# Optimization experiments

Measured on AMD Instinct MI355X. Metric: run time of the kernel, lower is better.

The kernel has to match this reference:

```python
import jax, jax.numpy as jnp
import numpy as np

K = 20
EPS = 1e-5

def _lrelu(x):
    return jnp.where(x >= 0, x, 0.2 * x)

def _bn(x, g, b, m, v, axis=1):
    shp = [1] * x.ndim
    shp[axis] = -1
    scale = (g / jnp.sqrt(v + EPS)).reshape(shp)
    return (x - m.reshape(shp)) * scale + b.reshape(shp)

def _graph_feature(x, k):
    # x: [B, C, N] -> [B, 2C, N, k]  (kNN in feature space, concat(x_j - x_i, x_i))
    xx = jnp.sum(x * x, axis=1)                        # [B, N]
    inner = jnp.einsum('bcn,bcm->bnm', x, x)           # [B, N, N]
    neg_dist = 2.0 * inner - xx[:, :, None] - xx[:, None, :]
    _, idx = jax.lax.top_k(neg_dist, k)                # [B, N, k] nearest neighbors
    xt = jnp.transpose(x, (0, 2, 1))                   # [B, N, C]
    nb = jax.vmap(lambda f, i: f[i])(xt, idx)          # [B, N, k, C]
    center = jnp.broadcast_to(xt[:, :, None, :], nb.shape)
    feat = jnp.concatenate([nb - center, center], axis=-1)  # [B, N, k, 2C]
    return jnp.transpose(feat, (0, 3, 1, 2))

def _edge_block(x, w, g, b, m, v):
    # EdgeConv: graph feature -> 1x1 conv -> BN -> LeakyReLU -> max over k
    f = _graph_feature(x, K)                           # [B, 2C, N, k]
    y = jnp.einsum('oc,bcnk->bonk', w, f)
    y = _lrelu(_bn(y, g, b, m, v, 1))
    return jnp.max(y, axis=-1)                         # [B, O, N]


def setup_inputs() -> dict:
    key = jax.random.key(0)
    ks = iter(jax.random.split(key, 64))
    def randn(*s, scale=1.0):
        return jax.random.normal(next(ks), s, dtype=jnp.float32) * scale
    def unif(*s):
        return jax.random.uniform(next(ks), s, dtype=jnp.float32, minval=0.5, maxval=1.5)
    d = {}
    d['x'] = randn(16, 3, 1024)
    # conv / linear weights (fan-in scaled)
    for name, o, c in [('w1', 64, 6), ('w2', 64, 128), ('w3', 128, 128),
                       ('w4', 256, 256), ('w5', 1024, 512),
                       ('wl1', 512, 2048), ('wl2', 256, 512), ('wl3', 101, 256)]:
        d[name] = randn(o, c, scale=1.0 / np.sqrt(c))
    d['bl2'] = randn(256, scale=0.02)
    d['bl3'] = randn(101, scale=0.02)
    # BN params (eval-mode running stats)
    for i, c in [('1', 64), ('2', 64), ('3', 128), ('4', 256), ('5', 1024), ('6', 512), ('7', 256)]:
        d['g' + i] = 1.0 + randn(c, scale=0.1)
        d['b' + i] = randn(c, scale=0.1)
        d['m' + i] = randn(c, scale=0.1)
        d['v' + i] = unif(c)
    return d


def reference(x, w1, g1, b1, m1, v1, w2, g2, b2, m2, v2, w3, g3, b3, m3, v3,
              w4, g4, b4, m4, v4, w5, g5, b5, m5, v5,
              wl1, g6, b6, m6, v6, wl2, bl2, g7, b7, m7, v7, wl3, bl3):
    x1 = _edge_block(x,  w1, g1, b1, m1, v1)   # [B, 64, N]
    x2 = _edge_block(x1, w2, g2, b2, m2, v2)   # [B, 64, N]
    x3 = _edge_block(x2, w3, g3, b3, m3, v3)   # [B, 128, N]
    x4 = _edge_block(x3, w4, g4, b4, m4, v4)   # [B, 256, N]
    xc = jnp.concatenate([x1, x2, x3, x4], axis=1)           # [B, 512, N]
    y = _lrelu(_bn(jnp.einsum('oc,bcn->bon', w5, xc), g5, b5, m5, v5, 1))  # [B, 1024, N]
    p = jnp.concatenate([jnp.max(y, axis=-1), jnp.mean(y, axis=-1)], axis=1)  # [B, 2048]
    h = _lrelu(_bn(p @ wl1.T, g6, b6, m6, v6, 1))            # [B, 512]
    h = _lrelu(_bn(h @ wl2.T + bl2, g7, b7, m7, v7, 1))      # [B, 256]
    return h @ wl3.T + bl3                                   # [B, 101]
```

## Files before the change

### kernel.cpp

```cpp
#include <hip/hip_runtime.h>
#include <cstdint>
#include <cmath>

#define DI __device__ __forceinline__

constexpr int BB = 16;
constexpr int NN = 1024;
constexpr int KK = 20;
constexpr int NPT = BB*NN;
constexpr float EPSF = 1e-5f;
constexpr float NEGINF = -3.0e38f;

DI float lrelu(float x){ return x >= 0.f ? x : 0.2f * x; }
DI float dot4(const float4 a, const float4 b){ return a.x*b.x + a.y*b.y + a.z*b.z + a.w*b.w; }
DI unsigned short f2bf(float x){
    uint32_t u = __float_as_uint(x);
    uint32_t r = (u + 0x7fffu + ((u >> 16) & 1u)) >> 16;
    return (unsigned short)r;
}

typedef __attribute__((ext_vector_type(8))) short short8v;
typedef __attribute__((ext_vector_type(4))) float f32x4;

__global__ void k_transpose(const float* __restrict__ x, float* __restrict__ xt)
{
    int i = blockIdx.x * 256 + threadIdx.x;
    if (i >= NPT) return;
    int b = i >> 10, n = i & 1023;
    #pragma unroll
    for (int c = 0; c < 3; ++c) xt[i*3 + c] = x[(b*3 + c)*NN + n];
}

__global__ void k_sqnorm(const float* __restrict__ src, int stride, int C, float* __restrict__ xx)
{
    int i = blockIdx.x * 256 + threadIdx.x;
    if (i >= NPT) return;
    const float* r = src + (size_t)i * stride;
    float s = 0.f;
    for (int c = 0; c < C; ++c){ float v = r[c]; s += v * v; }
    xx[i] = s;
}

template<int C>
__global__ __launch_bounds__(1024, 4) void k_knn(const float* __restrict__ src, int stride,
                                                 const float* __restrict__ xx,
                                                 int* __restrict__ idxo)
{
    constexpr bool SMALL = (C == 3);
    constexpr int CG = SMALL ? 1 : (C / 4);
    constexpr int TS = SMALL ? 5 : C;
    __shared__ float tile[128 * TS];

    const int tid  = threadIdx.x;
    const int lane = tid & 63;
    const int wv   = __builtin_amdgcn_readfirstlane(tid >> 6);
    const int b  = blockIdx.x >> 4;
    const int q0 = (blockIdx.x & 15) << 6;
    const int qbase = b*NN + q0 + (wv << 2);

    const float* qp0 = src + (size_t)(qbase + 0)*stride;
    const float* qp1 = src + (size_t)(qbase + 1)*stride;
    const float* qp2 = src + (size_t)(qbase + 2)*stride;
    const float* qp3 = src + (size_t)(qbase + 3)*stride;

    float xxq[4];
    #pragma unroll
    for (int q = 0; q < 4; ++q) xxq[q] = xx[qbase + q];

    float val[4][16];

    #pragma unroll
    for (int t = 0; t < 8; ++t){
        __syncthreads();
        if constexpr (SMALL){
            for (int i = tid; i < 128*3; i += 1024){
                int row = i / 3, c = i % 3;
                tile[row*TS + c] = src[(size_t)(b*NN + t*128 + row)*stride + c];
            }
        } else {
            for (int i = tid; i < 128*CG; i += 1024){
                int row = i / CG, cg = i % CG;
                int p = cg ^ (row & (CG - 1));
                float4 v = *(const float4*)(src + (size_t)(b*NN + t*128 + row)*stride + cg*4);
                *(float4*)(tile + row*TS + p*4) = v;
            }
        }
        __syncthreads();

        float acc[4][2];
        #pragma unroll
        for (int q = 0; q < 4; ++q){ acc[q][0] = 0.f; acc[q][1] = 0.f; }

        if constexpr (SMALL){
            float c0a = tile[lane*TS+0], c0b = tile[lane*TS+1], c0c = tile[lane*TS+2];
            float c1a = tile[(64+lane)*TS+0], c1b = tile[(64+lane)*TS+1], c1c = tile[(64+lane)*TS+2];
            float q00 = qp0[0], q01 = qp0[1], q02 = qp0[2];
            float q10 = qp1[0], q11 = qp1[1], q12 = qp1[2];
            float q20 = qp2[0], q21 = qp2[1], q22 = qp2[2];
            float q30 = qp3[0], q31 = qp3[1], q32 = qp3[2];
            acc[0][0] = q00*c0a + q01*c0b + q02*c0c;  acc[0][1] = q00*c1a + q01*c1b + q02*c1c;
            acc[1][0] = q10*c0a + q11*c0b + q12*c0c;  acc[1][1] = q10*c1a + q11*c1b + q12*c1c;
            acc[2][0] = q20*c0a + q21*c0b + q22*c0c;  acc[2][1] = q20*c1a + q21*c1b + q22*c1c;
            acc[3][0] = q30*c0a + q31*c0b + q32*c0c;  acc[3][1] = q30*c1a + q31*c1b + q32*c1c;
        } else {
            const int sw = lane & (CG - 1);
            #pragma unroll 2
            for (int cg0 = 0; cg0 < CG; ++cg0){
                float4 cf0 = *(const float4*)(tile + lane*TS      + ((cg0 ^ sw) << 2));
                float4 cf1 = *(const float4*)(tile + (64+lane)*TS + ((cg0 ^ sw) << 2));
                float4 qf0 = *(const float4*)(qp0 + (cg0 << 2));
                float4 qf1 = *(const float4*)(qp1 + (cg0 << 2));
                float4 qf2 = *(const float4*)(qp2 + (cg0 << 2));
                float4 qf3 = *(const float4*)(qp3 + (cg0 << 2));
                acc[0][0] += dot4(qf0, cf0); acc[0][1] += dot4(qf0, cf1);
                acc[1][0] += dot4(qf1, cf0); acc[1][1] += dot4(qf1, cf1);
                acc[2][0] += dot4(qf2, cf0); acc[2][1] += dot4(qf2, cf1);
                acc[3][0] += dot4(qf3, cf0); acc[3][1] += dot4(qf3, cf1);
            }
        }
        float xxm0 = xx[b*NN + t*128 + lane];
        float xxm1 = xx[b*NN + t*128 + 64 + lane];
        #pragma unroll
        for (int q = 0; q < 4; ++q){
            val[q][2*t]   = 2.f*acc[q][0] - xxq[q] - xxm0;
            val[q][2*t+1] = 2.f*acc[q][1] - xxq[q] - xxm1;
        }
    }

    #pragma unroll
    for (int q = 0; q < 4; ++q){
        const int orow = (qbase + q) * KK;

        float s[16];
        #pragma unroll
        for (int j = 0; j < 16; ++j) s[j] = val[q][j];
        #pragma unroll
        for (int k = 2; k <= 16; k <<= 1){
            #pragma unroll
            for (int jj = k >> 1; jj > 0; jj >>= 1){
                #pragma unroll
                for (int i = 0; i < 16; ++i){
                    int l = i ^ jj;
                    if (l > i){
                        float a = s[i], c = s[l];
                        float mx = fmaxf(a, c), mn = fminf(a, c);
                        bool up = ((i & k) == 0);
                        s[i] = up ? mx : mn;
                        s[l] = up ? mn : mx;
                    }
                }
            }
        }

        float T = NEGINF;
        for (int it = 0; it < 21; ++it){
            float m = s[0];
            #pragma unroll
            for (int d = 1; d < 64; d <<= 1) m = fmaxf(m, __shfl_xor(m, d));
            T = m;
            unsigned long long mk = __ballot(s[0] == m);
            int wl = __ffsll(mk) - 1;
            bool adv = (lane == wl);
            #pragma unroll
            for (int j = 0; j < 15; ++j) s[j] = adv ? s[j+1] : s[j];
            s[15] = adv ? NEGINF : s[15];
        }

        int cnt = 0;
        #pragma unroll
        for (int j = 0; j < 16; ++j) cnt += (val[q][j] > T) ? 1 : 0;
        int off = cnt;
        #pragma unroll
        for (int d = 1; d < 64; d <<= 1){
            int tt = __shfl_up(off, d);
            if (lane >= d) off += tt;
        }
        int total = __shfl(off, 63);
        int pos = orow + off - cnt;
        #pragma unroll
        for (int j = 0; j < 16; ++j){
            if (val[q][j] > T){ idxo[pos] = j*64 + lane; ++pos; }
        }
        if (total < KK){
            int rem = KK - total;
            int prior = 0;
            #pragma unroll
            for (int j = 0; j < 16; ++j){
                unsigned long long mk = __ballot(val[q][j] == T);
                int below = __popcll(mk & ((1ull << lane) - 1ull));
                if ((val[q][j] == T) && (prior + below < rem))
                    idxo[orow + total + prior + below] = j*64 + lane;
                prior += __popcll(mk);
            }
        }
    }
}

__global__ void k_wprep(const float* __restrict__ w, int O, int C, float* __restrict__ wp)
{
    int i = blockIdx.x*256 + threadIdx.x;
    if (i >= O*C) return;
    int o = i / C, c = i % C;
    float a = w[o*2*C + c];
    float bq = w[o*2*C + C + c];
    wp[o*C + c]       = a;
    wp[(O + o)*C + c] = bq - a;
}

template<int K, int M2, int O>
__global__ __launch_bounds__(256) void k_uvgemm(const float* __restrict__ srcp,
    const float* __restrict__ wp,
    const float* __restrict__ g, const float* __restrict__ bp,
    const float* __restrict__ mp, const float* __restrict__ vp,
    float* __restrict__ ub, float* __restrict__ xcv)
{
    constexpr int LD = 136;
    __shared__ float wl[16*LD];
    __shared__ float xl[16*LD];
    const int tid = threadIdx.x;
    const int nt = blockIdx.x & 127;
    const int mt = blockIdx.x >> 7;
    const int to = tid >> 4, tn = tid & 15;

    float acc[8][8];
    #pragma unroll
    for (int i = 0; i < 8; ++i)
        #pragma unroll
        for (int j = 0; j < 8; ++j) acc[i][j] = 0.f;

    for (int c0 = 0; c0 < K; c0 += 16){
        __syncthreads();
        #pragma unroll
        for (int p = 0; p < 2; ++p){
            int fi = tid + (p << 8);
            int row = fi >> 2, cq = (fi & 3) << 2;
            float4 wv = *(const float4*)(wp + (size_t)(mt*128 + row)*K + c0 + cq);
            wl[(cq+0)*LD + row] = wv.x;
            wl[(cq+1)*LD + row] = wv.y;
            wl[(cq+2)*LD + row] = wv.z;
            wl[(cq+3)*LD + row] = wv.w;
            float4 xv = *(const float4*)(srcp + (size_t)(nt*128 + row)*512 + c0 + cq);
            xl[(cq+0)*LD + row] = xv.x;
            xl[(cq+1)*LD + row] = xv.y;
            xl[(cq+2)*LD + row] = xv.z;
            xl[(cq+3)*LD + row] = xv.w;
        }
        __syncthreads();
        #pragma unroll
        for (int cc = 0; cc < 16; ++cc){
            float4 a0 = *(const float4*)(wl + cc*LD + to*8);
            float4 a1 = *(const float4*)(wl + cc*LD + to*8 + 4);
            float4 b0 = *(const float4*)(xl + cc*LD + tn*8);
            float4 b1 = *(const float4*)(xl + cc*LD + tn*8 + 4);
            float av[8] = {a0.x,a0.y,a0.z,a0.w,a1.x,a1.y,a1.z,a1.w};
            float bv[8] = {b0.x,b0.y,b0.z,b0.w,b1.x,b1.y,b1.z,b1.w};
            #pragma unroll
            for (int i = 0; i < 8; ++i)
                #pragma unroll
                for (int j = 0; j < 8; ++j) acc[i][j] += av[i]*bv[j];
        }
    }

    const int mbase = mt*128 + to*8;
    const bool isu = mbase < O;
    float mult[8], add[8];
    #pragma unroll
    for (int i = 0; i < 8; ++i){
        int m = mbase + i;
        if (isu){
            float s = g[m] / sqrtf(vp[m] + EPSF);
            mult[i] = (s >= 0.f) ? 1.f : -1.f;
            add[i]  = 0.f;
        } else {
            int o = m - O;
            float s = g[o] / sqrtf(vp[o] + EPSF);
            mult[i] = s;
            add[i]  = bp[o] - mp[o]*s;
        }
    }
    #pragma unroll
    for (int j = 0; j < 8; ++j){
        int pt = nt*128 + tn*8 + j;
        float4 v0, v1;
        v0.x = fmaf(mult[0], acc[0][j], add[0]);
        v0.y = fmaf(mult[1], acc[1][j], add[1]);
        v0.z = fmaf(mult[2], acc[2][j], add[2]);
        v0.w = fmaf(mult[3], acc[3][j], add[3]);
        v1.x = fmaf(mult[4], acc[4][j], add[4]);
        v1.y = fmaf(mult[5], acc[5][j], add[5]);
        v1.z = fmaf(mult[6], acc[6][j], add[6]);
        v1.w = fmaf(mult[7], acc[7][j], add[7]);
        if (isu){
            float* d = ub + (size_t)pt*O + mbase;
            *(float4*)(d)     = v0;
            *(float4*)(d + 4) = v1;
        } else {
            float* d = xcv + (size_t)pt*512 + (mbase - O);
            *(float4*)(d)     = v0;
            *(float4*)(d + 4) = v1;
        }
    }
}

__global__ __launch_bounds__(256) void k_uv3(const float* __restrict__ xt,
    const float* __restrict__ wp,
    const float* __restrict__ g, const float* __restrict__ bp,
    const float* __restrict__ mp, const float* __restrict__ vp,
    float* __restrict__ ub, float* __restrict__ xcv)
{
    __shared__ float wpl[128*3];
    __shared__ float mult[128], add[128];
    const int tid = threadIdx.x;
    if (tid < 128){
        int m = tid;
        if (m < 64){
            float s = g[m] / sqrtf(vp[m] + EPSF);
            mult[m] = (s >= 0.f) ? 1.f : -1.f;
            add[m]  = 0.f;
        } else {
            int o = m - 64;
            float s = g[o] / sqrtf(vp[o] + EPSF);
            mult[m] = s;
            add[m]  = bp[o] - mp[o]*s;
        }
    }
    for (int i = tid; i < 128*3; i += 256) wpl[i] = wp[i];
    __syncthreads();

    const int ptl = tid >> 5, mg = tid & 31;
    const int m0 = mg * 4;
    const int pt = blockIdx.x*8 + ptl;
    float x0 = xt[pt*3+0], x1 = xt[pt*3+1], x2 = xt[pt*3+2];
    float4 v4;
    float tmp[4];
    #pragma unroll
    for (int r = 0; r < 4; ++r){
        int m = m0 + r;
        float a = wpl[m*3+0]*x0 + wpl[m*3+1]*x1 + wpl[m*3+2]*x2;
        tmp[r] = fmaf(mult[m], a, add[m]);
    }
    v4.x = tmp[0]; v4.y = tmp[1]; v4.z = tmp[2]; v4.w = tmp[3];
    if (m0 < 64) *(float4*)(ub + (size_t)pt*64 + m0) = v4;
    else         *(float4*)(xcv + (size_t)pt*512 + (m0 - 64)) = v4;
}

template<int O>
__global__ __launch_bounds__(256) void k_edgemax(const float* __restrict__ ub,
    const int* __restrict__ idxg,
    const float* __restrict__ g, const float* __restrict__ vp,
    float* __restrict__ xcv)
{
    constexpr int TPP = O / 4;
    constexpr int PPB = 256 / TPP;
    const int tid = threadIdx.x;
    const int pt  = blockIdx.x*PPB + tid / TPP;
    const int oq  = (tid % TPP) * 4;
    const int bb  = pt & ~(NN-1);

    int nb[KK];
    #pragma unroll
    for (int k = 0; k < KK; ++k) nb[k] = idxg[pt*KK + k];

    float4 mx = *(const float4*)(ub + (size_t)(bb + nb[0])*O + oq);
    #pragma unroll
    for (int k = 1; k < KK; ++k){
        float4 u = *(const float4*)(ub + (size_t)(bb + nb[k])*O + oq);
        mx.x = fmaxf(mx.x, u.x); mx.y = fmaxf(mx.y, u.y);
        mx.z = fmaxf(mx.z, u.z); mx.w = fmaxf(mx.w, u.w);
    }
    float4 gv = *(const float4*)(g + oq);
    float4 vv = *(const float4*)(vp + oq);
    float4 as;
    as.x = fabsf(gv.x / sqrtf(vv.x + EPSF));
    as.y = fabsf(gv.y / sqrtf(vv.y + EPSF));
    as.z = fabsf(gv.z / sqrtf(vv.z + EPSF));
    as.w = fabsf(gv.w / sqrtf(vv.w + EPSF));
    float* d = xcv + (size_t)pt*512 + oq;
    float4 vr = *(const float4*)(d);
    float4 y;
    y.x = lrelu(fmaf(as.x, mx.x, vr.x));
    y.y = lrelu(fmaf(as.y, mx.y, vr.y));
    y.z = lrelu(fmaf(as.z, mx.z, vr.z));
    y.w = lrelu(fmaf(as.w, mx.w, vr.w));
    *(float4*)(d) = y;
}

__global__ void k_castbf(const float* __restrict__ s, unsigned short* __restrict__ d, int n8)
{
    int i = blockIdx.x*256 + threadIdx.x;
    if (i >= n8) return;
    const float4* sp = (const float4*)s + (size_t)i*2;
    float4 a = sp[0], b = sp[1];
    union { unsigned short u[8]; uint4 v; } o;
    o.u[0] = f2bf(a.x); o.u[1] = f2bf(a.y); o.u[2] = f2bf(a.z); o.u[3] = f2bf(a.w);
    o.u[4] = f2bf(b.x); o.u[5] = f2bf(b.y); o.u[6] = f2bf(b.z); o.u[7] = f2bf(b.w);
    *((uint4*)d + i) = o.v;
}

__global__ __launch_bounds__(256) void k_conv5mfma(const unsigned short* __restrict__ xcb,
    const unsigned short* __restrict__ w5b,
    const float* __restrict__ g, const float* __restrict__ bp,
    const float* __restrict__ mp, const float* __restrict__ vp,
    float* __restrict__ pmax, float* __restrict__ psum)
{
    __shared__ __align__(16) short lA[128*32];
    __shared__ __align__(16) short lB[128*32];
    __shared__ float scl[128], adl[128];
    __shared__ float red[2][128][2];

    const int tid = threadIdx.x;
    const int lane = tid & 63, wave = tid >> 6;
    const int wm = wave >> 1, wn = wave & 1;
    const int b  = blockIdx.x >> 6;
    const int mt = (blockIdx.x >> 3) & 7;
    const int nt = blockIdx.x & 7;

    if (tid < 128){
        int o = mt*128 + tid;
        float s = g[o] / sqrtf(vp[o] + EPSF);
        scl[tid] = s;
        adl[tid] = bp[o] - mp[o]*s;
    }

    f32x4 acc[4][4];
    #pragma unroll
    for (int i = 0; i < 4; ++i)
        #pragma unroll
        for (int j = 0; j < 4; ++j) acc[i][j] = (f32x4){0.f,0.f,0.f,0.f};

    const unsigned short* gA = w5b + (size_t)(mt*128)*512;
    const unsigned short* gB = xcb + (size_t)(b*1024 + nt*128)*512;

    for (int ks = 0; ks < 16; ++ks){
        __syncthreads();
        #pragma unroll
        for (int p = 0; p < 2; ++p){
            int off = p*256 + tid;
            int row = off >> 2;
            int slot = off & 3;
            int ssl = slot ^ (row & 3);
            *(uint4*)(lA + row*32 + ssl*8) = *(const uint4*)(gA + (size_t)row*512 + ks*32 + slot*8);
            *(uint4*)(lB + row*32 + ssl*8) = *(const uint4*)(gB + (size_t)row*512 + ks*32 + slot*8);
        }
        __syncthreads();

        short8v afr[4], bfr[4];
        #pragma unroll
        for (int i = 0; i < 4; ++i){
            int row = wm*64 + i*16 + (lane & 15);
            int sl  = (lane >> 4) ^ (row & 3);
            afr[i] = *(const short8v*)(lA + row*32 + sl*8);
        }
        #pragma unroll
        for (int j = 0; j < 4; ++j){
            int row = wn*64 + j*16 + (lane & 15);
            int sl  = (lane >> 4) ^ (row & 3);
            bfr[j] = *(const short8v*)(lB + row*32 + sl*8);
        }
        #pragma unroll
        for (int i = 0; i < 4; ++i)
            #pragma unroll
            for (int j = 0; j < 4; ++j)
                acc[i][j] = __builtin_amdgcn_mfma_f32_16x16x32_bf16(afr[i], bfr[j], acc[i][j], 0, 0, 0);
    }

    float emx[4][4], esm[4][4];
    #pragma unroll
    for (int i = 0; i < 4; ++i){
        #pragma unroll
        for (int r = 0; r < 4; ++r){
            int m_loc = wm*64 + i*16 + (lane >> 4)*4 + r;
            float s = scl[m_loc], t = adl[m_loc];
            float mx = NEGINF, sm = 0.f;
            #pragma unroll
            for (int j = 0; j < 4; ++j){
                float y = lrelu(fmaf(acc[i][j][r], s, t));
                mx = fmaxf(mx, y); sm += y;
            }
            #pragma unroll
            for (int d = 1; d < 16; d <<= 1){
                mx = fmaxf(mx, __shfl_xor(mx, d));
                sm += __shfl_xor(sm, d);
            }
            emx[i][r] = mx; esm[i][r] = sm;
        }
    }
    if ((lane & 15) == 0){
        #pragma unroll
        for (int i = 0; i < 4; ++i)
            #pragma unroll
            for (int r = 0; r < 4; ++r){
                int m_loc = wm*64 + i*16 + (lane >> 4)*4 + r;
                red[wn][m_loc][0] = emx[i][r];
                red[wn][m_loc][1] = esm[i][r];
            }
    }
    __syncthreads();
    if (tid < 128){
        float mx = fmaxf(red[0][tid][0], red[1][tid][0]);
        float sm = red[0][tid][1] + red[1][tid][1];
        int o = mt*128 + tid;
        pmax[(size_t)(b*NN + o)*8 + nt] = mx;
        psum[(size_t)(b*NN + o)*8 + nt] = sm;
    }
}

__global__ void k_poolfin(const float* __restrict__ pmax, const float* __restrict__ psum,
                          float* __restrict__ p)
{
    int i = blockIdx.x*256 + threadIdx.x;
    if (i >= NPT) return;
    int b = i >> 10, o = i & 1023;
    float mx = NEGINF, sm = 0.f;
    #pragma unroll
    for (int t = 0; t < 8; ++t){ mx = fmaxf(mx, pmax[(size_t)i*8 + t]); sm += psum[(size_t)i*8 + t]; }
    p[b*2048 + o]        = mx;
    p[b*2048 + 1024 + o] = sm * (1.f/1024.f);
}

template<int IN, int O, bool HASBN, bool HASBIAS>
__global__ void k_fc(const float* __restrict__ in, const float* __restrict__ W,
                     const float* __restrict__ bias,
                     const float* __restrict__ g, const float* __restrict__ bp,
                     const float* __restrict__ mp, const float* __restrict__ vp,
                     float* __restrict__ out)
{
    int i = blockIdx.x*256 + threadIdx.x;
    if (i >= BB*O) return;
    int b = i / O, o = i % O;
    const float* wr = W  + (size_t)o*IN;
    const float* ir = in + (size_t)b*IN;
    float s = 0.f;
    #pragma unroll 4
    for (int c = 0; c < IN; c += 4){
        float4 a = *(const float4*)(wr + c);
        float4 x = *(const float4*)(ir + c);
        s += dot4(a, x);
    }
    if (HASBIAS) s += bias[o];
    if (HASBN){
        float sc = g[o] / sqrtf(vp[o] + EPSF);
        s = (s - mp[o])*sc + bp[o];
        s = lrelu(s);
    }
    out[(size_t)b*O + o] = s;
}

extern "C" void kernel_launch(void* const* d_in, const int* in_sizes, int n_in,
                              void* d_out, int out_size, void* d_ws, size_t ws_size,
                              hipStream_t stream)
{
    (void)in_sizes; (void)n_in; (void)out_size; (void)ws_size;
    const float* x   = (const float*)d_in[0];
    const float* w1  = (const float*)d_in[1];
    const float* w2  = (const float*)d_in[2];
    const float* w3  = (const float*)d_in[3];
    const float* w4  = (const float*)d_in[4];
    const float* w5  = (const float*)d_in[5];
    const float* wl1 = (const float*)d_in[6];
    const float* wl2 = (const float*)d_in[7];
    const float* wl3 = (const float*)d_in[8];
    const float* bl2 = (const float*)d_in[9];
    const float* bl3 = (const float*)d_in[10];
    const float* g1 = (const float*)d_in[11]; const float* b1 = (const float*)d_in[12];
    const float* m1 = (const float*)d_in[13]; const float* v1 = (const float*)d_in[14];
    const float* g2 = (const float*)d_in[15]; const float* b2 = (const float*)d_in[16];
    const float* m2 = (const float*)d_in[17]; const float* v2 = (const float*)d_in[18];
    const float* g3 = (const float*)d_in[19]; const float* b3 = (const float*)d_in[20];
    const float* m3 = (const float*)d_in[21]; const float* v3 = (const float*)d_in[22];
    const float* g4 = (const float*)d_in[23]; const float* b4 = (const float*)d_in[24];
    const float* m4 = (const float*)d_in[25]; const float* v4 = (const float*)d_in[26];
    const float* g5 = (const float*)d_in[27]; const float* b5 = (const float*)d_in[28];
    const float* m5 = (const float*)d_in[29]; const float* v5 = (const float*)d_in[30];
    const float* g6 = (const float*)d_in[31]; const float* b6 = (const float*)d_in[32];
    const float* m6 = (const float*)d_in[33]; const float* v6 = (const float*)d_in[34];
    const float* g7 = (const float*)d_in[35]; const float* b7 = (const float*)d_in[36];
    const float* m7 = (const float*)d_in[37]; const float* v7 = (const float*)d_in[38];

    float* wsf  = (float*)d_ws;
    float* xt0  = wsf;
    float* xc   = xt0 + 49152;
    float* xx   = xc + 8388608;
    int*   idx  = (int*)(xx + 16384);
    float* pmax = (float*)(idx + 327680);
    float* psum = pmax + 131072;
    float* p    = psum + 131072;
    float* h1   = p + 32768;
    float* h2   = h1 + 8192;
    float* ub   = h2 + 4096;
    float* wp   = ub + 4194304;
    unsigned short* xcb = (unsigned short*)ub;
    unsigned short* w5b = (unsigned short*)idx;

    k_transpose<<<64, 256, 0, stream>>>(x, xt0);

    k_sqnorm<<<64, 256, 0, stream>>>(xt0, 3, 3, xx);
    k_knn<3><<<256, 1024, 0, stream>>>(xt0, 3, xx, idx);
    k_wprep<<<1, 256, 0, stream>>>(w1, 64, 3, wp);
    k_uv3<<<2048, 256, 0, stream>>>(xt0, wp, g1, b1, m1, v1, ub, xc);
    k_edgemax<64><<<1024, 256, 0, stream>>>(ub, idx, g1, v1, xc);

    k_sqnorm<<<64, 256, 0, stream>>>(xc, 512, 64, xx);
    k_knn<64><<<256, 1024, 0, stream>>>(xc, 512, xx, idx);
    k_wprep<<<16, 256, 0, stream>>>(w2, 64, 64, wp);
    k_uvgemm<64, 128, 64><<<128, 256, 0, stream>>>(xc, wp, g2, b2, m2, v2, ub, xc + 64);
    k_edgemax<64><<<1024, 256, 0, stream>>>(ub, idx, g2, v2, xc + 64);

    k_sqnorm<<<64, 256, 0, stream>>>(xc + 64, 512, 64, xx);
    k_knn<64><<<256, 1024, 0, stream>>>(xc + 64, 512, xx, idx);
    k_wprep<<<32, 256, 0, stream>>>(w3, 128, 64, wp);
    k_uvgemm<64, 256, 128><<<256, 256, 0, stream>>>(xc + 64, wp, g3, b3, m3, v3, ub, xc + 128);
    k_edgemax<128><<<2048, 256, 0, stream>>>(ub, idx, g3, v3, xc + 128);

    k_sqnorm<<<64, 256, 0, stream>>>(xc + 128, 512, 128, xx);
    k_knn<128><<<256, 1024, 0, stream>>>(xc + 128, 512, xx, idx);
    k_wprep<<<128, 256, 0, stream>>>(w4, 256, 128, wp);
    k_uvgemm<128, 512, 256><<<512, 256, 0, stream>>>(xc + 128, wp, g4, b4, m4, v4, ub, xc + 256);
    k_edgemax<256><<<4096, 256, 0, stream>>>(ub, idx, g4, v4, xc + 256);

    k_castbf<<<4096, 256, 0, stream>>>(xc, xcb, 1048576);
    k_castbf<<<256, 256, 0, stream>>>(w5, w5b, 65536);
    k_conv5mfma<<<1024, 256, 0, stream>>>(xcb, w5b, g5, b5, m5, v5, pmax, psum);
    k_poolfin<<<64, 256, 0, stream>>>(pmax, psum, p);

    k_fc<2048, 512, true,  false><<<32, 256, 0, stream>>>(p,  wl1, nullptr, g6, b6, m6, v6, h1);
    k_fc<512,  256, true,  true ><<<16, 256, 0, stream>>>(h1, wl2, bl2,     g7, b7, m7, v7, h2);
    k_fc<256,  101, false, true ><<<7,  256, 0, stream>>>(h2, wl3, bl3, nullptr, nullptr, nullptr, nullptr, (float*)d_out);
}
```

Baseline: 612.0 us.

## Interleave two kNN query rows in selection and store layer-4 edge terms as bf16

The kNN selection now handles two query rows per pass. Their bitonic sorts, shuffle reductions and ballots are interleaved, giving the scheduler independent work to hide shuffle latency. Separately, the layer-4 neighbor term buffer is written as bf16 and read back with 8-byte loads in the edge-max kernel. This halves the gather traffic in that kernel. The cost is higher register pressure in kNN and reduced precision of the neighbor-max values in layer 4.

```diff
diff --git a/kernel.cpp b/kernel.cpp
--- a/kernel.cpp
+++ b/kernel.cpp
@@ -128,12 +128,11 @@
     }
 
     #pragma unroll
-    for (int q = 0; q < 4; ++q){
-        const int orow = (qbase + q) * KK;
-
-        float s[16];
-        #pragma unroll
-        for (int j = 0; j < 16; ++j) s[j] = val[q][j];
+    for (int qq = 0; qq < 4; qq += 2){
+        float s0[16], s1[16];
+        #pragma unroll
+        for (int j = 0; j < 16; ++j){ s0[j] = val[qq][j]; s1[j] = val[qq+1][j]; }
+
         #pragma unroll
         for (int k = 2; k <= 16; k <<= 1){
             #pragma unroll
@@ -142,55 +141,73 @@
                 for (int i = 0; i < 16; ++i){
                     int l = i ^ jj;
                     if (l > i){
-                        float a = s[i], c = s[l];
-                        float mx = fmaxf(a, c), mn = fminf(a, c);
                         bool up = ((i & k) == 0);
-                        s[i] = up ? mx : mn;
-                        s[l] = up ? mn : mx;
+                        float a0 = s0[i], c0 = s0[l];
+                        float mx0 = fmaxf(a0, c0), mn0 = fminf(a0, c0);
+                        s0[i] = up ? mx0 : mn0;  s0[l] = up ? mn0 : mx0;
+                        float a1 = s1[i], c1 = s1[l];
+                        float mx1 = fmaxf(a1, c1), mn1 = fminf(a1, c1);
+                        s1[i] = up ? mx1 : mn1;  s1[l] = up ? mn1 : mx1;
                     }
                 }
             }
         }
 
-        float T = NEGINF;
+        float T0 = NEGINF, T1 = NEGINF;
         for (int it = 0; it < 21; ++it){
-            float m = s[0];
-            #pragma unroll
-            for (int d = 1; d < 64; d <<= 1) m = fmaxf(m, __shfl_xor(m, d));
-            T = m;
-            unsigned long long mk = __ballot(s[0] == m);
-            int wl = __ffsll(mk) - 1;
-            bool adv = (lane == wl);
-            #pragma unroll
-            for (int j = 0; j < 15; ++j) s[j] = adv ? s[j+1] : s[j];
-            s[15] = adv ? NEGINF : s[15];
-        }
-
-        int cnt = 0;
-        #pragma unroll
-        for (int j = 0; j < 16; ++j) cnt += (val[q][j] > T) ? 1 : 0;
-        int off = cnt;
-        #pragma unroll
-        for (int d = 1; d < 64; d <<= 1){
-            int tt = __shfl_up(off, d);
-            if (lane >= d) off += tt;
-        }
-        int total = __shfl(off, 63);
-        int pos = orow + off - cnt;
-        #pragma unroll
-        for (int j = 0; j < 16; ++j){
-            if (val[q][j] > T){ idxo[pos] = j*64 + lane; ++pos; }
-        }
-        if (total < KK){
-            int rem = KK - total;
-            int prior = 0;
+            float m0 = s0[0], m1 = s1[0];
+            #pragma unroll
+            for (int d = 1; d < 64; d <<= 1){
+                float p0 = __shfl_xor(m0, d);
+                float p1 = __shfl_xor(m1, d);
+                m0 = fmaxf(m0, p0);
+                m1 = fmaxf(m1, p1);
+            }
+            T0 = m0; T1 = m1;
+            unsigned long long mk0 = __ballot(s0[0] == m0);
+            unsigned long long mk1 = __ballot(s1[0] == m1);
+            bool a0 = (lane == __ffsll(mk0) - 1);
+            bool a1 = (lane == __ffsll(mk1) - 1);
+            #pragma unroll
+            for (int j = 0; j < 15; ++j){
+                s0[j] = a0 ? s0[j+1] : s0[j];
+                s1[j] = a1 ? s1[j+1] : s1[j];
+            }
+            s0[15] = a0 ? NEGINF : s0[15];
+            s1[15] = a1 ? NEGINF : s1[15];
+        }
+
+        #pragma unroll
+        for (int h = 0; h < 2; ++h){
+            const int q = qq + h;
+            const float T = h ? T1 : T0;
+            const int orow = (qbase + q) * KK;
+            int cnt = 0;
+            #pragma unroll
+            for (int j = 0; j < 16; ++j) cnt += (val[q][j] > T) ? 1 : 0;
+            int off = cnt;
+            #pragma unroll
+            for (int d = 1; d < 64; d <<= 1){
+                int tt = __shfl_up(off, d);
+                if (lane >= d) off += tt;
+            }
+            int total = __shfl(off, 63);
+            int pos = orow + off - cnt;
             #pragma unroll
             for (int j = 0; j < 16; ++j){
-                unsigned long long mk = __ballot(val[q][j] == T);
-                int below = __popcll(mk & ((1ull << lane) - 1ull));
-                if ((val[q][j] == T) && (prior + below < rem))
-                    idxo[orow + total + prior + below] = j*64 + lane;
-                prior += __popcll(mk);
+                if (val[q][j] > T){ idxo[pos] = j*64 + lane; ++pos; }
+            }
+            if (total < KK){
+                int rem = KK - total;
+                int prior = 0;
+                #pragma unroll
+                for (int j = 0; j < 16; ++j){
+                    unsigned long long mk = __ballot(val[q][j] == T);
+                    int below = __popcll(mk & ((1ull << lane) - 1ull));
+                    if ((val[q][j] == T) && (prior + below < rem))
+                        idxo[orow + total + prior + below] = j*64 + lane;
+                    prior += __popcll(mk);
+                }
             }
         }
     }
@@ -207,7 +224,7 @@
     wp[(O + o)*C + c] = bq - a;
 }
 
-template<int K, int M2, int O>
+template<int K, int M2, int O, bool UB16>
 __global__ __launch_bounds__(256) void k_uvgemm(const float* __restrict__ srcp,
     const float* __restrict__ wp,
     const float* __restrict__ g, const float* __restrict__ bp,
@@ -291,9 +308,16 @@
         v1.z = fmaf(mult[6], acc[6][j], add[6]);
         v1.w = fmaf(mult[7], acc[7][j], add[7]);
         if (isu){
-            float* d = ub + (size_t)pt*O + mbase;
-            *(float4*)(d)     = v0;
-            *(float4*)(d + 4) = v1;
+            if constexpr (UB16){
+                union { unsigned short u[8]; uint4 v; } o;
+                o.u[0] = f2bf(v0.x); o.u[1] = f2bf(v0.y); o.u[2] = f2bf(v0.z); o.u[3] = f2bf(v0.w);
+                o.u[4] = f2bf(v1.x); o.u[5] = f2bf(v1.y); o.u[6] = f2bf(v1.z); o.u[7] = f2bf(v1.w);
+                *(uint4*)((unsigned short*)ub + (size_t)pt*O + mbase) = o.v;
+            } else {
+                float* d = ub + (size_t)pt*O + mbase;
+                *(float4*)(d)     = v0;
+                *(float4*)(d + 4) = v1;
+            }
         } else {
             float* d = xcv + (size_t)pt*512 + (mbase - O);
             *(float4*)(d)     = v0;
@@ -344,7 +368,7 @@
     else         *(float4*)(xcv + (size_t)pt*512 + (m0 - 64)) = v4;
 }
 
-template<int O>
+template<int O, bool UB16>
 __global__ __launch_bounds__(256) void k_edgemax(const float* __restrict__ ub,
     const int* __restrict__ idxg,
     const float* __restrict__ g, const float* __restrict__ vp,
@@ -361,12 +385,30 @@
     #pragma unroll
     for (int k = 0; k < KK; ++k) nb[k] = idxg[pt*KK + k];
 
-    float4 mx = *(const float4*)(ub + (size_t)(bb + nb[0])*O + oq);
-    #pragma unroll
-    for (int k = 1; k < KK; ++k){
-        float4 u = *(const float4*)(ub + (size_t)(bb + nb[k])*O + oq);
-        mx.x = fmaxf(mx.x, u.x); mx.y = fmaxf(mx.y, u.y);
-        mx.z = fmaxf(mx.z, u.z); mx.w = fmaxf(mx.w, u.w);
+    float4 mx;
+    if constexpr (UB16){
+        const unsigned short* ubh = (const unsigned short*)ub;
+        uint2 r0 = *(const uint2*)(ubh + (size_t)(bb + nb[0])*O + oq);
+        mx.x = __uint_as_float(r0.x << 16);
+        mx.y = __uint_as_float(r0.x & 0xffff0000u);
+        mx.z = __uint_as_float(r0.y << 16);
+        mx.w = __uint_as_float(r0.y & 0xffff0000u);
+        #pragma unroll
+        for (int k = 1; k < KK; ++k){
+            uint2 r = *(const uint2*)(ubh + (size_t)(bb + nb[k])*O + oq);
+            mx.x = fmaxf(mx.x, __uint_as_float(r.x << 16));
+            mx.y = fmaxf(mx.y, __uint_as_float(r.x & 0xffff0000u));
+            mx.z = fmaxf(mx.z, __uint_as_float(r.y << 16));
+            mx.w = fmaxf(mx.w, __uint_as_float(r.y & 0xffff0000u));
+        }
+    } else {
+        mx = *(const float4*)(ub + (size_t)(bb + nb[0])*O + oq);
+        #pragma unroll
+        for (int k = 1; k < KK; ++k){
+            float4 u = *(const float4*)(ub + (size_t)(bb + nb[k])*O + oq);
+            mx.x = fmaxf(mx.x, u.x); mx.y = fmaxf(mx.y, u.y);
+            mx.z = fmaxf(mx.z, u.z); mx.w = fmaxf(mx.w, u.w);
+        }
     }
     float4 gv = *(const float4*)(g + oq);
     float4 vv = *(const float4*)(vp + oq);
@@ -598,25 +640,25 @@
     k_knn<3><<<256, 1024, 0, stream>>>(xt0, 3, xx, idx);
     k_wprep<<<1, 256, 0, stream>>>(w1, 64, 3, wp);
     k_uv3<<<2048, 256, 0, stream>>>(xt0, wp, g1, b1, m1, v1, ub, xc);
-    k_edgemax<64><<<1024, 256, 0, stream>>>(ub, idx, g1, v1, xc);
+    k_edgemax<64, false><<<1024, 256, 0, stream>>>(ub, idx, g1, v1, xc);
 
     k_sqnorm<<<64, 256, 0, stream>>>(xc, 512, 64, xx);
     k_knn<64><<<256, 1024, 0, stream>>>(xc, 512, xx, idx);
     k_wprep<<<16, 256, 0, stream>>>(w2, 64, 64, wp);
-    k_uvgemm<64, 128, 64><<<128, 256, 0, stream>>>(xc, wp, g2, b2, m2, v2, ub, xc + 64);
-    k_edgemax<64><<<1024, 256, 0, stream>>>(ub, idx, g2, v2, xc + 64);
+    k_uvgemm<64, 128, 64, false><<<128, 256, 0, stream>>>(xc, wp, g2, b2, m2, v2, ub, xc + 64);
+    k_edgemax<64, false><<<1024, 256, 0, stream>>>(ub, idx, g2, v2, xc + 64);
 
     k_sqnorm<<<64, 256, 0, stream>>>(xc + 64, 512, 64, xx);
     k_knn<64><<<256, 1024, 0, stream>>>(xc + 64, 512, xx, idx);
     k_wprep<<<32, 256, 0, stream>>>(w3, 128, 64, wp);
-    k_uvgemm<64, 256, 128><<<256, 256, 0, stream>>>(xc + 64, wp, g3, b3, m3, v3, ub, xc + 128);
-    k_edgemax<128><<<2048, 256, 0, stream>>>(ub, idx, g3, v3, xc + 128);
+    k_uvgemm<64, 256, 128, false><<<256, 256, 0, stream>>>(xc + 64, wp, g3, b3, m3, v3, ub, xc + 128);
+    k_edgemax<128, false><<<2048, 256, 0, stream>>>(ub, idx, g3, v3, xc + 128);
 
     k_sqnorm<<<64, 256, 0, stream>>>(xc + 128, 512, 128, xx);
     k_knn<128><<<256, 1024, 0, stream>>>(xc + 128, 512, xx, idx);
     k_wprep<<<128, 256, 0, stream>>>(w4, 256, 128, wp);
-    k_uvgemm<128, 512, 256><<<512, 256, 0, stream>>>(xc + 128, wp, g4, b4, m4, v4, ub, xc + 256);
-    k_edgemax<256><<<4096, 256, 0, stream>>>(ub, idx, g4, v4, xc + 256);
+    k_uvgemm<128, 512, 256, true><<<512, 256, 0, stream>>>(xc + 128, wp, g4, b4, m4, v4, ub, xc + 256);
+    k_edgemax<256, true><<<4096, 256, 0, stream>>>(ub, idx, g4, v4, xc + 256);
 
     k_castbf<<<4096, 256, 0, stream>>>(xc, xcb, 1048576);
     k_castbf<<<256, 256, 0, stream>>>(w5, w5b, 65536);
```

Result: no change. 619.5 us (+1.2%).
